# Kernel tuning notes

Hardware: AMD Instinct MI355X
Metric: run time of the kernel (lower is better)

Reference implementation:

```python
import jax, jax.numpy as jnp
import numpy as np

BATCH, FIELD0, EMB = 1024, 32, 64
LAYER_SIZES = (128, 128, 128)  # split_half=True -> hidden field sizes [32, 64, 64]


def setup_inputs() -> dict:
    key = jax.random.key(0)
    ks = jax.random.split(key, 7)
    x = jax.random.normal(ks[0], (BATCH, FIELD0, EMB), dtype=jnp.float32)
    # Conv1D(kernel_size=1) weights: (in_channels=f0*fi, filters=layer_size), plus bias.
    field_sizes = [FIELD0]
    params = {}
    for i, size in enumerate(LAYER_SIZES):
        fi = field_sizes[-1]
        fan_in = FIELD0 * fi
        scale = 1.0 / np.sqrt(fan_in)
        params[f"W{i}"] = jax.random.normal(ks[1 + 2 * i], (fan_in, size), dtype=jnp.float32) * scale
        params[f"b{i}"] = jnp.zeros((size,), dtype=jnp.float32)
        field_sizes.append(size // 2 if i != len(LAYER_SIZES) - 1 else size)
    return {"x": x, **params}


def reference(x, W0, b0, W1, b1, W2, b2):
    # CIN: outer product + 1x1 conv (a matmul over the flattened field-pair axis)
    # fused as a single bilinear contraction per layer:
    #   cur[b,k,e] = sum_{i,j} x[b,i,e] * hidden[b,j,e] * W[i,j,k] + b[k]
    Ws = [(W0, b0), (W1, b1), (W2, b2)]
    f0 = x.shape[1]
    hidden = x
    final_outputs = []
    n_layers = len(Ws)
    for idx, (W, b) in enumerate(Ws):
        fi = hidden.shape[1]
        Wr = W.reshape(f0, fi, W.shape[-1])  # channel m = i*fi + j (row-major reshape)
        cur = jnp.einsum('bie,bje,ijk->bke', x, hidden, Wr) + b[None, :, None]
        # activation=None -> linear
        if idx != n_layers - 1:
            half = cur.shape[1] // 2
            hidden, direct = cur[:, :half, :], cur[:, half:, :]
        else:
            direct = cur
        final_outputs.append(direct)
    result = jnp.concatenate(final_outputs, axis=1)  # (B, 64+64+128, E)
    return jnp.sum(result, axis=-1)  # (B, 256)
```

## Files before the change

kernel.cpp:

```cpp
#include <hip/hip_runtime.h>
#include <hip/hip_bf16.h>
#include <cstdint>


typedef _Float16 half8  __attribute__((ext_vector_type(8)));
typedef _Float16 half4_ __attribute__((ext_vector_type(4)));
typedef _Float16 half2_ __attribute__((ext_vector_type(2)));
typedef float    f32x4  __attribute__((ext_vector_type(4)));

__device__ __forceinline__ unsigned short f16bits(float v) {
    return __builtin_bit_cast(unsigned short, (_Float16)v);
}

__global__ void pack_w_all(const float* __restrict__ W0, _Float16* __restrict__ Wt0,
                           const float* __restrict__ W1, _Float16* __restrict__ Wt1,
                           const float* __restrict__ W2, _Float16* __restrict__ Wt2)
{
    __shared__ _Float16 ldsT[128 * 33];
    const int blk = blockIdx.x, t = threadIdx.x;
    const float* W;
    _Float16* Wt;
    int c;
    if (blk < 32)       { W = W0; Wt = Wt0; c = blk; }
    else if (blk < 96)  { W = W1; Wt = Wt1; c = blk - 32; }
    else                { W = W2; Wt = Wt2; c = blk - 96; }

    for (int p = t; p < 32 * 128; p += 256) {
        int kk = p >> 7, m = p & 127;
        ldsT[m * 33 + kk] = (_Float16)W[(size_t)(c * 32 + kk) * 128 + m];
    }
    __syncthreads();
    int m = t >> 1, kk0 = (t & 1) * 16;
    half8 v0, v1;
#pragma unroll
    for (int i = 0; i < 8; ++i) {
        v0[i] = ldsT[m * 33 + kk0 + i];
        v1[i] = ldsT[m * 33 + kk0 + 8 + i];
    }
    *(half8*)(Wt + (size_t)c * 4096 + t * 16)     = v0;
    *(half8*)(Wt + (size_t)c * 4096 + t * 16 + 8) = v1;
}

__global__ __launch_bounds__(256, 2)
void cin_fused(const float* __restrict__ x,
               const _Float16* __restrict__ Wt0,
               const _Float16* __restrict__ Wt1,
               const float* __restrict__ bs0,
               const float* __restrict__ bs1,
               _Float16* __restrict__ S0,
               _Float16* __restrict__ S1,
               _Float16* __restrict__ S2)
{
    __shared__ alignas(16) char smem[61440];
    _Float16* slotA = (_Float16*)smem;
    _Float16* slotB = (_Float16*)(smem + 18432);
    _Float16* sX    = (_Float16*)(smem + 36864);
    _Float16* xchg  = (_Float16*)(smem + 45056);

    const int t = threadIdx.x, lane = t & 63, w = t >> 6;
    const int ks = w & 1, bb = w >> 1;
    const int lr = lane & 15, q = lane >> 4;
    const int b0 = blockIdx.x * 2;
    const int batch = b0 + bb;

    {
        const float4* xv = (const float4*)(x + (size_t)b0 * 2048);
#pragma unroll
        for (int s = 0; s < 4; ++s) {
            int p4 = t + s * 256;
            float4 v = xv[p4];
            int bb2 = p4 >> 9, idx = (p4 & 511) * 4;
            int i = idx >> 6, e0 = idx & 63;
            _Float16 h0 = (_Float16)v.x, h1 = (_Float16)v.y;
            _Float16 h2 = (_Float16)v.z, h3 = (_Float16)v.w;
            half4_ pk = {h0, h1, h2, h3};
            *(half4_*)(sX + bb2 * 2048 + i * 64 + e0) = pk;
            _Float16* hb = slotA + bb2 * 2560;
            hb[(e0 + 0) * 40 + i] = h0;
            hb[(e0 + 1) * 40 + i] = h1;
            hb[(e0 + 2) * 40 + i] = h2;
            hb[(e0 + 3) * 40 + i] = h3;
        }
    }
    __syncthreads();

    f32x4 acc[4][4];

    auto kloop = [&](const _Float16* WtL, int cBeg, int cEnd, int ish,
                     const _Float16* hbase, int ph) {
#pragma unroll
        for (int mt = 0; mt < 4; ++mt)
#pragma unroll
            for (int nt = 0; nt < 4; ++nt)
                acc[mt][nt] = f32x4{0.0f, 0.0f, 0.0f, 0.0f};
        const _Float16* aG = WtL + lr * 32 + q * 8;
        const _Float16* hP = hbase + bb * (ph << 6) + lr * ph + q * 8;
        const _Float16* xP = sX + bb * 2048 + lr;
        half8 afA[4], afB[4], hvA[4], hvB[4];
        _Float16 xsA[4], xsB[4];
        auto pf = [&](half8* af, half8* hv, _Float16* xs, int c) {
            const int i  = c >> ish;
            const int j0 = (c - (i << ish)) << 5;
            const _Float16* ag = aG + (size_t)c * 4096;
#pragma unroll
            for (int mt = 0; mt < 4; ++mt) af[mt] = *(const half8*)(ag + mt * 512);
#pragma unroll
            for (int nt = 0; nt < 4; ++nt) {
                hv[nt] = *(const half8*)(hP + nt * (ph << 4) + j0);
                xs[nt] = xP[(i << 6) + (nt << 4)];
            }
        };
        auto cp = [&](half8* af, half8* hv, _Float16* xs) {
#pragma unroll
            for (int nt = 0; nt < 4; ++nt) {
                half2_ xv2 = {xs[nt], xs[nt]};
                half8 xv8 = __builtin_shufflevector(xv2, xv2, 0, 1, 0, 1, 0, 1, 0, 1);
                half8 bf = hv[nt] * xv8;
#pragma unroll
                for (int mt = 0; mt < 4; ++mt)
                    acc[mt][nt] = __builtin_amdgcn_mfma_f32_16x16x32_f16(
                        af[mt], bf, acc[mt][nt], 0, 0, 0);
            }
        };
        pf(afA, hvA, xsA, cBeg);
        for (int c = cBeg; c < cEnd; c += 2) {
            pf(afB, hvB, xsB, c + 1);
            cp(afA, hvA, xsA);
            if (c + 2 < cEnd) pf(afA, hvA, xsA, c + 2);
            cp(afB, hvB, xsB);
        }
    };

    auto xchg_write = [&]() {
#pragma unroll
        for (int cc = 0; cc < 8; ++cc) {
            int mt = cc >> 1, n0 = (cc & 1) * 2;
            half8 hv8;
#pragma unroll
            for (int r = 0; r < 4; ++r) {
                hv8[r]     = (_Float16)acc[mt][n0][r];
                hv8[4 + r] = (_Float16)acc[mt][n0 + 1][r];
            }
            int sl = (cc + lane) & 7;
            *(half8*)(xchg + bb * 4096 + lane * 64 + sl * 8) = hv8;
        }
    };
    auto xchg_read = [&]() {
#pragma unroll
        for (int cc = 0; cc < 8; ++cc) {
            int mt = cc >> 1, n0 = (cc & 1) * 2;
            int sl = (cc + lane) & 7;
            half8 hv8 = *(const half8*)(xchg + bb * 4096 + lane * 64 + sl * 8);
#pragma unroll
            for (int r = 0; r < 4; ++r) {
                acc[mt][n0][r]     += (float)hv8[r];
                acc[mt][n0 + 1][r] += (float)hv8[4 + r];
            }
        }
    };

    auto sgemm = [&](const _Float16* hJ, int jp, int fi, _Float16* Sdst) {
        const _Float16* axp = sX + bb * 2048 + (ks * 16 + lr) * 64 + q * 8;
        const int njt = fi >> 4;
        for (int jt = 0; jt < njt; ++jt) {
            f32x4 sa = {0.0f, 0.0f, 0.0f, 0.0f};
#pragma unroll
            for (int c2 = 0; c2 < 2; ++c2) {
                half8 a = *(const half8*)(axp + c2 * 32);
                half8 b = *(const half8*)(hJ + (jt * 16 + lr) * jp + q * 8 + c2 * 32);
                sa = __builtin_amdgcn_mfma_f32_16x16x32_f16(a, b, sa, 0, 0, 0);
            }
#pragma unroll
            for (int r = 0; r < 4; ++r)
                Sdst[(size_t)batch * (32 * fi) + (ks * 16 + q * 4 + r) * fi
                     + jt * 16 + lr] = (_Float16)sa[r];
        }
    };

    sgemm(sX + bb * 2048, 64, 32, S0);
    kloop(Wt0, ks * 16, ks * 16 + 16, 0, slotA, 40);
    if (ks == 1) xchg_write();
    __syncthreads();
    if (ks == 0) {
        xchg_read();
#pragma unroll
        for (int mt = 0; mt < 4; ++mt)
#pragma unroll
            for (int nt = 0; nt < 4; ++nt) {
                int e = nt * 16 + lr;
                int j = mt * 16 + q * 4;
                half4_ vh;
#pragma unroll
                for (int r = 0; r < 4; ++r) {
                    _Float16 hval = (_Float16)(acc[mt][nt][r] + bs0[j + r]);
                    vh[r] = hval;
                    slotA[bb * 4608 + (j + r) * 72 + e] = hval;
                }
                *(half4_*)(slotB + bb * 4608 + e * 72 + j) = vh;
            }
    }
    __syncthreads();

    sgemm(slotA + bb * 4608, 72, 64, S1);
    kloop(Wt1, ks * 32, ks * 32 + 32, 1, slotB, 72);
    if (ks == 1) xchg_write();
    __syncthreads();
    if (ks == 0) {
        xchg_read();
#pragma unroll
        for (int mt = 0; mt < 4; ++mt)
#pragma unroll
            for (int nt = 0; nt < 4; ++nt) {
                int e = nt * 16 + lr;
                int j = mt * 16 + q * 4;
#pragma unroll
                for (int r = 0; r < 4; ++r)
                    slotA[bb * 4608 + (j + r) * 72 + e]
                        = (_Float16)(acc[mt][nt][r] + bs1[j + r]);
            }
    }
    __syncthreads();

    sgemm(slotA + bb * 4608, 72, 64, S2);
}

__global__ __launch_bounds__(256, 4)
void cin_direct(const _Float16* __restrict__ S0v, const _Float16* __restrict__ S1v,
                const _Float16* __restrict__ S2v,
                const _Float16* __restrict__ Wt0, const _Float16* __restrict__ Wt1,
                const _Float16* __restrict__ Wt2,
                const float* __restrict__ bs0, const float* __restrict__ bs1,
                const float* __restrict__ bs2,
                float* __restrict__ out)
{
    const int t = threadIdx.x, lane = t & 63;
    const int lr = lane & 15, q = lane >> 4;
    const int W = blockIdx.x * 4 + (t >> 6);

    const _Float16 *S, *Wt;
    const float* bias;
    int fan, nch, dm0, ob, idx;
    if (W < 256)      { S = S0v; Wt = Wt0; bias = bs0; fan = 1024; nch = 32; dm0 = 64; ob = 0;   idx = W; }
    else if (W < 512) { S = S1v; Wt = Wt1; bias = bs1; fan = 2048; nch = 64; dm0 = 64; ob = 64;  idx = W - 256; }
    else              { S = S2v; Wt = Wt2; bias = bs2; fan = 2048; nch = 64; dm0 = 0;  ob = 128; idx = W - 512; }
    const int bt = idx & 63, kt = idx >> 6;
    const int bbase = bt * 16;

    const _Float16* aG = Wt + (dm0 + kt * 16 + lr) * 32 + q * 8;
    const _Float16* bG = S + (size_t)(bbase + lr) * fan + q * 8;

    f32x4 acc = {0.0f, 0.0f, 0.0f, 0.0f};
    half8 aA = *(const half8*)(aG);
    half8 bA = *(const half8*)(bG);
    for (int c = 0; c < nch; c += 2) {
        half8 aB = *(const half8*)(aG + (size_t)(c + 1) * 4096);
        half8 bB = *(const half8*)(bG + (c + 1) * 32);
        acc = __builtin_amdgcn_mfma_f32_16x16x32_f16(aA, bA, acc, 0, 0, 0);
        if (c + 2 < nch) {
            aA = *(const half8*)(aG + (size_t)(c + 2) * 4096);
            bA = *(const half8*)(bG + (c + 2) * 32);
        }
        acc = __builtin_amdgcn_mfma_f32_16x16x32_f16(aB, bB, acc, 0, 0, 0);
    }
#pragma unroll
    for (int r = 0; r < 4; ++r) {
        int kl = kt * 16 + q * 4 + r;
        out[(size_t)(bbase + lr) * 256 + ob + kl] = acc[r] + 64.0f * bias[dm0 + kl];
    }
}

extern "C" void kernel_launch(void* const* d_in, const int* in_sizes, int n_in,
                              void* d_out, int out_size, void* d_ws, size_t ws_size,
                              hipStream_t stream)
{
    const float* x  = (const float*)d_in[0];
    const float* W0 = (const float*)d_in[1];
    const float* b0 = (const float*)d_in[2];
    const float* W1 = (const float*)d_in[3];
    const float* b1 = (const float*)d_in[4];
    const float* W2 = (const float*)d_in[5];
    const float* b2 = (const float*)d_in[6];
    float* out = (float*)d_out;

    char* ws = (char*)d_ws;
    _Float16* Wt0 = (_Float16*)(ws + 0);
    _Float16* Wt1 = (_Float16*)(ws + 262144);
    _Float16* Wt2 = (_Float16*)(ws + 786432);
    _Float16* S0  = (_Float16*)(ws + 1310720);
    _Float16* S1  = (_Float16*)(ws + 3407872);
    _Float16* S2  = (_Float16*)(ws + 7602176);
    (void)in_sizes; (void)n_in; (void)out_size; (void)ws_size;

    hipLaunchKernelGGL(pack_w_all, dim3(160), dim3(256), 0, stream,
                       W0, Wt0, W1, Wt1, W2, Wt2);

    hipLaunchKernelGGL(cin_fused, dim3(512), dim3(256), 0, stream,
                       x, Wt0, Wt1, b0, b1, S0, S1, S2);

    hipLaunchKernelGGL(cin_direct, dim3(256), dim3(256), 0, stream,
                       S0, S1, S2, Wt0, Wt1, Wt2, b0, b1, b2, out);
}
```

Before: 120.3 us.

## Split CIN work by output rows per batch and split-K the direct GEMM

Result: faster. 116.4 us (-3.2%).

```diff
diff --git a/kernel.cpp b/kernel.cpp
--- a/kernel.cpp
+++ b/kernel.cpp
@@ -1,5 +1,4 @@
 #include <hip/hip_runtime.h>
-#include <hip/hip_bf16.h>
 #include <cstdint>
 
 
@@ -7,10 +6,6 @@
 typedef _Float16 half4_ __attribute__((ext_vector_type(4)));
 typedef _Float16 half2_ __attribute__((ext_vector_type(2)));
 typedef float    f32x4  __attribute__((ext_vector_type(4)));
-
-__device__ __forceinline__ unsigned short f16bits(float v) {
-    return __builtin_bit_cast(unsigned short, (_Float16)v);
-}
 
 __global__ void pack_w_all(const float* __restrict__ W0, _Float16* __restrict__ Wt0,
                            const float* __restrict__ W1, _Float16* __restrict__ Wt1,
@@ -41,7 +36,7 @@
     *(half8*)(Wt + (size_t)c * 4096 + t * 16 + 8) = v1;
 }
 
-__global__ __launch_bounds__(256, 2)
+__global__ __launch_bounds__(128, 4)
 void cin_fused(const float* __restrict__ x,
                const _Float16* __restrict__ Wt0,
                const _Float16* __restrict__ Wt1,
@@ -51,59 +46,58 @@
                _Float16* __restrict__ S1,
                _Float16* __restrict__ S2)
 {
-    __shared__ alignas(16) char smem[61440];
-    _Float16* slotA = (_Float16*)smem;
-    _Float16* slotB = (_Float16*)(smem + 18432);
-    _Float16* sX    = (_Float16*)(smem + 36864);
-    _Float16* xchg  = (_Float16*)(smem + 45056);
-
-    const int t = threadIdx.x, lane = t & 63, w = t >> 6;
-    const int ks = w & 1, bb = w >> 1;
+    __shared__ alignas(16) char smem[22528];
+    _Float16* sX  = (_Float16*)smem;
+    _Float16* R_A = (_Float16*)(smem + 4096);
+    _Float16* R_B = (_Float16*)(smem + 13312);
+
+    const int t = threadIdx.x, lane = t & 63, ks = t >> 6;
     const int lr = lane & 15, q = lane >> 4;
-    const int b0 = blockIdx.x * 2;
-    const int batch = b0 + bb;
+    const int b = blockIdx.x;
 
     {
-        const float4* xv = (const float4*)(x + (size_t)b0 * 2048);
+        const float4* xv = (const float4*)(x + (size_t)b * 2048);
 #pragma unroll
         for (int s = 0; s < 4; ++s) {
-            int p4 = t + s * 256;
+            int p4 = t + s * 128;
             float4 v = xv[p4];
-            int bb2 = p4 >> 9, idx = (p4 & 511) * 4;
-            int i = idx >> 6, e0 = idx & 63;
+            int idx = p4 * 4, i = idx >> 6, e0 = idx & 63;
             _Float16 h0 = (_Float16)v.x, h1 = (_Float16)v.y;
             _Float16 h2 = (_Float16)v.z, h3 = (_Float16)v.w;
             half4_ pk = {h0, h1, h2, h3};
-            *(half4_*)(sX + bb2 * 2048 + i * 64 + e0) = pk;
-            _Float16* hb = slotA + bb2 * 2560;
-            hb[(e0 + 0) * 40 + i] = h0;
-            hb[(e0 + 1) * 40 + i] = h1;
-            hb[(e0 + 2) * 40 + i] = h2;
-            hb[(e0 + 3) * 40 + i] = h3;
-        }
-    }
-    __syncthreads();
-
-    f32x4 acc[4][4];
-
-    auto kloop = [&](const _Float16* WtL, int cBeg, int cEnd, int ish,
-                     const _Float16* hbase, int ph) {
-#pragma unroll
-        for (int mt = 0; mt < 4; ++mt)
+            *(half4_*)(sX + i * 64 + e0) = pk;
+            *(half4_*)(R_B + i * 72 + e0) = pk;
+            R_A[(e0 + 0) * 40 + i] = h0;
+            R_A[(e0 + 1) * 40 + i] = h1;
+            R_A[(e0 + 2) * 40 + i] = h2;
+            R_A[(e0 + 3) * 40 + i] = h3;
+        }
+    }
+    __syncthreads();
+
+    const half8 aF0 = *(const half8*)(R_B + (ks * 16 + lr) * 72 + q * 8);
+    const half8 aF1 = *(const half8*)(R_B + (ks * 16 + lr) * 72 + q * 8 + 32);
+
+    f32x4 acc[2][4];
+
+    auto kloop = [&](const _Float16* WtL, int nch, int ish,
+                     const _Float16* hb, int ph) {
+#pragma unroll
+        for (int mt = 0; mt < 2; ++mt)
 #pragma unroll
             for (int nt = 0; nt < 4; ++nt)
                 acc[mt][nt] = f32x4{0.0f, 0.0f, 0.0f, 0.0f};
-        const _Float16* aG = WtL + lr * 32 + q * 8;
-        const _Float16* hP = hbase + bb * (ph << 6) + lr * ph + q * 8;
-        const _Float16* xP = sX + bb * 2048 + lr;
-        half8 afA[4], afB[4], hvA[4], hvB[4];
+        const _Float16* aG = WtL + (ks * 32 + lr) * 32 + q * 8;
+        const _Float16* hP = hb + lr * ph + q * 8;
+        const _Float16* xP = sX + lr;
+        half8 afA[2], afB[2], hvA[4], hvB[4];
         _Float16 xsA[4], xsB[4];
         auto pf = [&](half8* af, half8* hv, _Float16* xs, int c) {
             const int i  = c >> ish;
             const int j0 = (c - (i << ish)) << 5;
             const _Float16* ag = aG + (size_t)c * 4096;
-#pragma unroll
-            for (int mt = 0; mt < 4; ++mt) af[mt] = *(const half8*)(ag + mt * 512);
+            af[0] = *(const half8*)(ag);
+            af[1] = *(const half8*)(ag + 512);
 #pragma unroll
             for (int nt = 0; nt < 4; ++nt) {
                 hv[nt] = *(const half8*)(hP + nt * (ph << 4) + j0);
@@ -116,115 +110,73 @@
                 half2_ xv2 = {xs[nt], xs[nt]};
                 half8 xv8 = __builtin_shufflevector(xv2, xv2, 0, 1, 0, 1, 0, 1, 0, 1);
                 half8 bf = hv[nt] * xv8;
-#pragma unroll
-                for (int mt = 0; mt < 4; ++mt)
-                    acc[mt][nt] = __builtin_amdgcn_mfma_f32_16x16x32_f16(
-                        af[mt], bf, acc[mt][nt], 0, 0, 0);
+                acc[0][nt] = __builtin_amdgcn_mfma_f32_16x16x32_f16(
+                    af[0], bf, acc[0][nt], 0, 0, 0);
+                acc[1][nt] = __builtin_amdgcn_mfma_f32_16x16x32_f16(
+                    af[1], bf, acc[1][nt], 0, 0, 0);
             }
         };
-        pf(afA, hvA, xsA, cBeg);
-        for (int c = cBeg; c < cEnd; c += 2) {
+        pf(afA, hvA, xsA, 0);
+        for (int c = 0; c < nch; c += 2) {
             pf(afB, hvB, xsB, c + 1);
             cp(afA, hvA, xsA);
-            if (c + 2 < cEnd) pf(afA, hvA, xsA, c + 2);
+            if (c + 2 < nch) pf(afA, hvA, xsA, c + 2);
             cp(afB, hvB, xsB);
         }
     };
 
-    auto xchg_write = [&]() {
-#pragma unroll
-        for (int cc = 0; cc < 8; ++cc) {
-            int mt = cc >> 1, n0 = (cc & 1) * 2;
-            half8 hv8;
-#pragma unroll
-            for (int r = 0; r < 4; ++r) {
-                hv8[r]     = (_Float16)acc[mt][n0][r];
-                hv8[4 + r] = (_Float16)acc[mt][n0 + 1][r];
-            }
-            int sl = (cc + lane) & 7;
-            *(half8*)(xchg + bb * 4096 + lane * 64 + sl * 8) = hv8;
-        }
-    };
-    auto xchg_read = [&]() {
-#pragma unroll
-        for (int cc = 0; cc < 8; ++cc) {
-            int mt = cc >> 1, n0 = (cc & 1) * 2;
-            int sl = (cc + lane) & 7;
-            half8 hv8 = *(const half8*)(xchg + bb * 4096 + lane * 64 + sl * 8);
-#pragma unroll
-            for (int r = 0; r < 4; ++r) {
-                acc[mt][n0][r]     += (float)hv8[r];
-                acc[mt][n0 + 1][r] += (float)hv8[4 + r];
-            }
-        }
-    };
-
-    auto sgemm = [&](const _Float16* hJ, int jp, int fi, _Float16* Sdst) {
-        const _Float16* axp = sX + bb * 2048 + (ks * 16 + lr) * 64 + q * 8;
+    auto sgemm = [&](const _Float16* hJ, int fi, _Float16* Sdst) {
         const int njt = fi >> 4;
         for (int jt = 0; jt < njt; ++jt) {
             f32x4 sa = {0.0f, 0.0f, 0.0f, 0.0f};
-#pragma unroll
-            for (int c2 = 0; c2 < 2; ++c2) {
-                half8 a = *(const half8*)(axp + c2 * 32);
-                half8 b = *(const half8*)(hJ + (jt * 16 + lr) * jp + q * 8 + c2 * 32);
-                sa = __builtin_amdgcn_mfma_f32_16x16x32_f16(a, b, sa, 0, 0, 0);
+            half8 bv0 = *(const half8*)(hJ + (jt * 16 + lr) * 72 + q * 8);
+            half8 bv1 = *(const half8*)(hJ + (jt * 16 + lr) * 72 + q * 8 + 32);
+            sa = __builtin_amdgcn_mfma_f32_16x16x32_f16(aF0, bv0, sa, 0, 0, 0);
+            sa = __builtin_amdgcn_mfma_f32_16x16x32_f16(aF1, bv1, sa, 0, 0, 0);
+#pragma unroll
+            for (int r = 0; r < 4; ++r)
+                Sdst[(size_t)b * (32 * fi) + (ks * 16 + q * 4 + r) * fi
+                     + jt * 16 + lr] = (_Float16)sa[r];
+        }
+    };
+
+    auto epi = [&](const float* bs, _Float16* hJ, _Float16* hT, bool wantT) {
+#pragma unroll
+        for (int mt = 0; mt < 2; ++mt) {
+            const int jb = ks * 32 + mt * 16 + q * 4;
+            const float b0f = bs[jb + 0], b1f = bs[jb + 1];
+            const float b2f = bs[jb + 2], b3f = bs[jb + 3];
+#pragma unroll
+            for (int nt = 0; nt < 4; ++nt) {
+                const int e = nt * 16 + lr;
+                half4_ vh;
+                vh[0] = (_Float16)(acc[mt][nt][0] + b0f);
+                vh[1] = (_Float16)(acc[mt][nt][1] + b1f);
+                vh[2] = (_Float16)(acc[mt][nt][2] + b2f);
+                vh[3] = (_Float16)(acc[mt][nt][3] + b3f);
+                hJ[(jb + 0) * 72 + e] = vh[0];
+                hJ[(jb + 1) * 72 + e] = vh[1];
+                hJ[(jb + 2) * 72 + e] = vh[2];
+                hJ[(jb + 3) * 72 + e] = vh[3];
+                if (wantT) *(half4_*)(hT + e * 72 + jb) = vh;
             }
-#pragma unroll
-            for (int r = 0; r < 4; ++r)
-                Sdst[(size_t)batch * (32 * fi) + (ks * 16 + q * 4 + r) * fi
-                     + jt * 16 + lr] = (_Float16)sa[r];
         }
     };
 
-    sgemm(sX + bb * 2048, 64, 32, S0);
-    kloop(Wt0, ks * 16, ks * 16 + 16, 0, slotA, 40);
-    if (ks == 1) xchg_write();
-    __syncthreads();
-    if (ks == 0) {
-        xchg_read();
-#pragma unroll
-        for (int mt = 0; mt < 4; ++mt)
-#pragma unroll
-            for (int nt = 0; nt < 4; ++nt) {
-                int e = nt * 16 + lr;
-                int j = mt * 16 + q * 4;
-                half4_ vh;
-#pragma unroll
-                for (int r = 0; r < 4; ++r) {
-                    _Float16 hval = (_Float16)(acc[mt][nt][r] + bs0[j + r]);
-                    vh[r] = hval;
-                    slotA[bb * 4608 + (j + r) * 72 + e] = hval;
-                }
-                *(half4_*)(slotB + bb * 4608 + e * 72 + j) = vh;
-            }
-    }
-    __syncthreads();
-
-    sgemm(slotA + bb * 4608, 72, 64, S1);
-    kloop(Wt1, ks * 32, ks * 32 + 32, 1, slotB, 72);
-    if (ks == 1) xchg_write();
-    __syncthreads();
-    if (ks == 0) {
-        xchg_read();
-#pragma unroll
-        for (int mt = 0; mt < 4; ++mt)
-#pragma unroll
-            for (int nt = 0; nt < 4; ++nt) {
-                int e = nt * 16 + lr;
-                int j = mt * 16 + q * 4;
-#pragma unroll
-                for (int r = 0; r < 4; ++r)
-                    slotA[bb * 4608 + (j + r) * 72 + e]
-                        = (_Float16)(acc[mt][nt][r] + bs1[j + r]);
-            }
-    }
-    __syncthreads();
-
-    sgemm(slotA + bb * 4608, 72, 64, S2);
-}
-
-__global__ __launch_bounds__(256, 4)
+    sgemm(R_B, 32, S0);
+    kloop(Wt0, 32, 0, R_A, 40);
+    __syncthreads();
+    epi(bs0, R_A, R_B, true);
+    __syncthreads();
+    sgemm(R_A, 64, S1);
+    kloop(Wt1, 64, 1, R_B, 72);
+    __syncthreads();
+    epi(bs1, R_B, nullptr, false);
+    __syncthreads();
+    sgemm(R_B, 64, S2);
+}
+
+__global__ __launch_bounds__(256, 2)
 void cin_direct(const _Float16* __restrict__ S0v, const _Float16* __restrict__ S1v,
                 const _Float16* __restrict__ S2v,
                 const _Float16* __restrict__ Wt0, const _Float16* __restrict__ Wt1,
@@ -233,39 +185,49 @@
                 const float* __restrict__ bs2,
                 float* __restrict__ out)
 {
-    const int t = threadIdx.x, lane = t & 63;
+    __shared__ f32x4 red[2][64];
+    const int t = threadIdx.x, lane = t & 63, w = t >> 6;
     const int lr = lane & 15, q = lane >> 4;
-    const int W = blockIdx.x * 4 + (t >> 6);
+    const int task = blockIdx.x * 2 + (w >> 1);
+    const int kh = w & 1;
 
     const _Float16 *S, *Wt;
     const float* bias;
     int fan, nch, dm0, ob, idx;
-    if (W < 256)      { S = S0v; Wt = Wt0; bias = bs0; fan = 1024; nch = 32; dm0 = 64; ob = 0;   idx = W; }
-    else if (W < 512) { S = S1v; Wt = Wt1; bias = bs1; fan = 2048; nch = 64; dm0 = 64; ob = 64;  idx = W - 256; }
-    else              { S = S2v; Wt = Wt2; bias = bs2; fan = 2048; nch = 64; dm0 = 0;  ob = 128; idx = W - 512; }
+    if (task < 256)      { S = S0v; Wt = Wt0; bias = bs0; fan = 1024; nch = 32; dm0 = 64; ob = 0;   idx = task; }
+    else if (task < 512) { S = S1v; Wt = Wt1; bias = bs1; fan = 2048; nch = 64; dm0 = 64; ob = 64;  idx = task - 256; }
+    else                 { S = S2v; Wt = Wt2; bias = bs2; fan = 2048; nch = 64; dm0 = 0;  ob = 128; idx = task - 512; }
     const int bt = idx & 63, kt = idx >> 6;
     const int bbase = bt * 16;
-
-    const _Float16* aG = Wt + (dm0 + kt * 16 + lr) * 32 + q * 8;
-    const _Float16* bG = S + (size_t)(bbase + lr) * fan + q * 8;
+    const int hn = nch >> 1, c0 = kh * hn;
+
+    const _Float16* aG = Wt + (size_t)(dm0 + kt * 16 + lr) * 32 + q * 8
+                            + (size_t)c0 * 4096;
+    const _Float16* bG = S + (size_t)(bbase + lr) * fan + q * 8 + c0 * 32;
 
     f32x4 acc = {0.0f, 0.0f, 0.0f, 0.0f};
     half8 aA = *(const half8*)(aG);
     half8 bA = *(const half8*)(bG);
-    for (int c = 0; c < nch; c += 2) {
+    for (int c = 0; c < hn; c += 2) {
         half8 aB = *(const half8*)(aG + (size_t)(c + 1) * 4096);
         half8 bB = *(const half8*)(bG + (c + 1) * 32);
         acc = __builtin_amdgcn_mfma_f32_16x16x32_f16(aA, bA, acc, 0, 0, 0);
-        if (c + 2 < nch) {
+        if (c + 2 < hn) {
             aA = *(const half8*)(aG + (size_t)(c + 2) * 4096);
             bA = *(const half8*)(bG + (c + 2) * 32);
         }
         acc = __builtin_amdgcn_mfma_f32_16x16x32_f16(aB, bB, acc, 0, 0, 0);
     }
-#pragma unroll
-    for (int r = 0; r < 4; ++r) {
-        int kl = kt * 16 + q * 4 + r;
-        out[(size_t)(bbase + lr) * 256 + ob + kl] = acc[r] + 64.0f * bias[dm0 + kl];
+    if (kh == 1) red[w >> 1][lane] = acc;
+    __syncthreads();
+    if (kh == 0) {
+        f32x4 o = red[w >> 1][lane];
+#pragma unroll
+        for (int r = 0; r < 4; ++r) {
+            int kl = kt * 16 + q * 4 + r;
+            out[(size_t)(bbase + lr) * 256 + ob + kl]
+                = acc[r] + o[r] + 64.0f * bias[dm0 + kl];
+        }
     }
 }
 
@@ -294,9 +256,9 @@
     hipLaunchKernelGGL(pack_w_all, dim3(160), dim3(256), 0, stream,
                        W0, Wt0, W1, Wt1, W2, Wt2);
 
-    hipLaunchKernelGGL(cin_fused, dim3(512), dim3(256), 0, stream,
+    hipLaunchKernelGGL(cin_fused, dim3(1024), dim3(128), 0, stream,
                        x, Wt0, Wt1, b0, b1, S0, S1, S2);
 
-    hipLaunchKernelGGL(cin_direct, dim3(256), dim3(256), 0, stream,
+    hipLaunchKernelGGL(cin_direct, dim3(512), dim3(256), 0, stream,
                        S0, S1, S2, Wt0, Wt1, Wt2, b0, b1, b2, out);
 }
```
